# Kernel optimization log

Measured on AMD Instinct MI355X. Metric: run time of the kernel, lower is better.

The kernel has to match this reference:

```python
import jax, jax.numpy as jnp
import numpy as np

DIM = 512
N_HEADS = 8
HEAD_DIM = DIM // N_HEADS
HID = 4 * DIM
N_LEVELS = 3  # len(chunk_sizes)
EPS = 1e-5


def layernorm(x, w, b):
    mu = jnp.mean(x, axis=-1, keepdims=True)
    var = jnp.var(x, axis=-1, keepdims=True)
    return (x - mu) * jax.lax.rsqrt(var + EPS) * w + b


def setup_inputs() -> dict:
    key = jax.random.key(0)
    ks = jax.random.split(key, 12)
    s = 1.0 / np.sqrt(DIM)
    sh = 1.0 / np.sqrt(HID)
    inp = {
        "x": jax.random.normal(ks[0], (4, 2048, DIM), dtype=jnp.float32),
        # torch nn.Linear stores weight as [out, in]; y = x @ W.T
        "Wq": jax.random.uniform(ks[1], (DIM, DIM), minval=-s, maxval=s),
        "Wk": jax.random.uniform(ks[2], (DIM, DIM), minval=-s, maxval=s),
        "Wv": jax.random.uniform(ks[3], (DIM, DIM), minval=-s, maxval=s),
        "Wo": jax.random.uniform(ks[4], (DIM, DIM), minval=-s, maxval=s),
        "ln1_w": jnp.ones((DIM,)), "ln1_b": jnp.zeros((DIM,)),
        "ln2_w": jnp.ones((DIM,)), "ln2_b": jnp.zeros((DIM,)),
        # CMS: per-level MLP, stored as [L, in, out]
        "cms_W1": jax.random.uniform(ks[5], (N_LEVELS, DIM, HID), minval=-s, maxval=s),
        "cms_b1": jnp.zeros((N_LEVELS, HID)),
        "cms_W2": jax.random.uniform(ks[6], (N_LEVELS, HID, DIM), minval=-sh, maxval=sh),
        "cms_b2": jnp.zeros((N_LEVELS, DIM)),
    }
    return inp


def self_mod_attn(h, Wq, Wk, Wv, Wo):
    B, S, _ = h.shape
    def split(y):  # [B,S,dim] -> [B,H,S,D]
        return y.reshape(B, S, N_HEADS, HEAD_DIM).transpose(0, 2, 1, 3)
    Q = split(h @ Wq.T)
    K = split(h @ Wk.T)
    V = split(h @ Wv.T)
    # per-step memory delta, mean over batch: U[h,s,d,k] = mean_b v_t k_t^T
    U = jnp.einsum("bhsd,bhsk->hsdk", V, K) / B
    # memory starts at zero (buffer) and accumulates INCLUDING step t before readout
    M = jnp.cumsum(U, axis=1)  # [H,S,D,D]
    y = jnp.einsum("hsdk,bhsk->bhsd", M, Q)  # readout
    y = y.transpose(0, 2, 1, 3).reshape(B, S, DIM)
    return y @ Wo.T


def cms(h, cms_W1, cms_b1, cms_W2, cms_b2):
    # sequential chain of per-level MLPs (dim -> 4*dim -> dim)
    for l in range(N_LEVELS):
        h = jax.nn.gelu(h @ cms_W1[l] + cms_b1[l]) @ cms_W2[l] + cms_b2[l]
    return h


def reference(x, Wq, Wk, Wv, Wo, ln1_w, ln1_b, ln2_w, ln2_b,
              cms_W1, cms_b1, cms_W2, cms_b2):
    x = x + self_mod_attn(layernorm(x, ln1_w, ln1_b), Wq, Wk, Wv, Wo)
    x = x + cms(layernorm(x, ln2_w, ln2_b), cms_W1, cms_b1, cms_W2, cms_b2)
    return x
```

## Files before the change

### kernel.cpp

```cpp
#include <hip/hip_runtime.h>
#include <hip/hip_bf16.h>
#include <cstdint>
#include <cstddef>

typedef __attribute__((ext_vector_type(8))) short bf16x8;
typedef __attribute__((ext_vector_type(4))) float f32x4;

#define MFMA16(a, b, c) __builtin_amdgcn_mfma_f32_16x16x32_bf16((a), (b), (c), 0, 0, 0)

static __device__ __forceinline__ unsigned short f2bf(float f) {
    union { float f; unsigned u; } v; v.f = f;
    unsigned r = v.u + 0x7fffu + ((v.u >> 16) & 1u);
    return (unsigned short)(r >> 16);
}

static __device__ __forceinline__ float gelu_tanh(float x) {
    float z = 0.7978845608028654f * (x + 0.044715f * x * x * x);
    float a = fabsf(z);
    float e = __expf(-2.0f * a);
    float t = (1.0f - e) / (1.0f + e);
    t = (z < 0.0f) ? -t : t;
    return 0.5f * x * (1.0f + t);
}

static __device__ __forceinline__ void gload16(const void* g, void* l) {
    __builtin_amdgcn_global_load_lds((const __attribute__((address_space(1))) unsigned int*)g,
                                     (__attribute__((address_space(3))) unsigned int*)l,
                                     16, 0, 0);
}

__global__ __launch_bounds__(256) void wcvt_kernel(const float* __restrict__ a, const float* __restrict__ b,
                                                   const float* __restrict__ c, const float* __restrict__ d,
                                                   unsigned short* __restrict__ o) {
    int i = blockIdx.x * 256 + threadIdx.x;
    int idx = i * 4;
    int which = idx >> 18;
    int off = idx & 262143;
    const float* src = (which == 0) ? a : (which == 1) ? b : (which == 2) ? c : d;
    float4 v = *(const float4*)(src + off);
    unsigned long long p = (unsigned long long)f2bf(v.x) | ((unsigned long long)f2bf(v.y) << 16)
                         | ((unsigned long long)f2bf(v.z) << 32) | ((unsigned long long)f2bf(v.w) << 48);
    *(unsigned long long*)(o + idx) = p;
}

__global__ __launch_bounds__(256) void wtrans_kernel(const float* __restrict__ in, unsigned short* __restrict__ out,
                                                     int R, int C) {
    __shared__ float tile[32][33];
    size_t lvl = blockIdx.z;
    in  += lvl * (size_t)R * C;
    out += lvl * (size_t)R * C;
    int c0 = blockIdx.x * 32, r0 = blockIdx.y * 32;
    int tx = threadIdx.x & 31, ty = threadIdx.x >> 5;
    #pragma unroll
    for (int ii = 0; ii < 4; ++ii) {
        int i = ty * 4 + ii;
        tile[i][tx] = in[(size_t)(r0 + i) * C + c0 + tx];
    }
    __syncthreads();
    #pragma unroll
    for (int jj = 0; jj < 4; ++jj) {
        int j = ty * 4 + jj;
        out[(size_t)(c0 + j) * R + r0 + tx] = f2bf(tile[tx][j]);
    }
}

__global__ __launch_bounds__(256) void ln_kernel(const float* __restrict__ x,
                                                 const float* __restrict__ w,
                                                 const float* __restrict__ b,
                                                 unsigned short* __restrict__ out) {
    int tid = threadIdx.x, l = tid & 63, wv = tid >> 6;
    size_t row = (size_t)blockIdx.x * 4 + wv;
    const float* xr = x + row * 512 + l * 8;
    float4 v0 = *(const float4*)xr;
    float4 v1 = *(const float4*)(xr + 4);
    float vv[8] = {v0.x, v0.y, v0.z, v0.w, v1.x, v1.y, v1.z, v1.w};
    float s = 0.f, q = 0.f;
    #pragma unroll
    for (int j = 0; j < 8; ++j) { s += vv[j]; q += vv[j] * vv[j]; }
    #pragma unroll
    for (int off = 1; off < 64; off <<= 1) { s += __shfl_xor(s, off); q += __shfl_xor(q, off); }
    float mu = s * (1.0f / 512.0f);
    float rs = rsqrtf(q * (1.0f / 512.0f) - mu * mu + 1e-5f);
    union { unsigned short us[8]; uint4 u; } pk;
    #pragma unroll
    for (int j = 0; j < 8; ++j)
        pk.us[j] = f2bf((vv[j] - mu) * rs * w[l * 8 + j] + b[l * 8 + j]);
    *(uint4*)(out + row * 512 + l * 8) = pk.u;
}

template<int EPI>
__global__ __launch_bounds__(256) void gemm_bt(
    const unsigned short* __restrict__ A,
    const unsigned short* __restrict__ Bt,
    int K, int N,
    unsigned short* __restrict__ outb,
    float* __restrict__ outf,
    const float* __restrict__ bias,
    const float* __restrict__ resid) {
    __shared__ bf16x8 As[1024];
    __shared__ bf16x8 Bs[1024];
    const int tid = threadIdx.x, l = tid & 63, w = tid >> 6;
    const int m0 = blockIdx.x * 128, n0 = blockIdx.y * 128;
    const int wr = (w >> 1) * 64, wc = (w & 1) * 64;
    const int srow = l >> 3;
    const int scol = ((l & 7) ^ srow) * 8;

    f32x4 acc[4][4] = {};
    const int nkt = K >> 6;
    for (int kt = 0; kt < nkt; ++kt) {
        const unsigned short* Ag = A + (size_t)m0 * K + kt * 64;
        const unsigned short* Bg = Bt + (size_t)n0 * K + kt * 64;
        #pragma unroll
        for (int i = 0; i < 4; ++i) {
            int chunk = i * 4 + w;
            int row = chunk * 8 + srow;
            gload16(Ag + (size_t)row * K + scol, &As[chunk * 64]);
            gload16(Bg + (size_t)row * K + scol, &Bs[chunk * 64]);
        }
        __syncthreads();
        #pragma unroll
        for (int kk = 0; kk < 2; ++kk) {
            bf16x8 af[4], bfr[4];
            #pragma unroll
            for (int mi = 0; mi < 4; ++mi) {
                int r = wr + mi * 16 + (l & 15);
                af[mi] = As[r * 8 + ((kk * 4 + (l >> 4)) ^ (r & 7))];
            }
            #pragma unroll
            for (int ni = 0; ni < 4; ++ni) {
                int r = wc + ni * 16 + (l & 15);
                bfr[ni] = Bs[r * 8 + ((kk * 4 + (l >> 4)) ^ (r & 7))];
            }
            #pragma unroll
            for (int mi = 0; mi < 4; ++mi)
                #pragma unroll
                for (int ni = 0; ni < 4; ++ni)
                    acc[mi][ni] = MFMA16(af[mi], bfr[ni], acc[mi][ni]);
        }
        __syncthreads();
    }
    #pragma unroll
    for (int mi = 0; mi < 4; ++mi)
        #pragma unroll
        for (int ni = 0; ni < 4; ++ni) {
            int col = n0 + wc + ni * 16 + (l & 15);
            #pragma unroll
            for (int r = 0; r < 4; ++r) {
                int row = m0 + wr + mi * 16 + (l >> 4) * 4 + r;
                float v = acc[mi][ni][r];
                size_t idx = (size_t)row * N + col;
                if constexpr (EPI == 0) {
                    outb[idx] = f2bf(v);
                } else if constexpr (EPI == 1) {
                    outf[idx] = v + resid[idx];
                } else if constexpr (EPI == 2) {
                    v += bias[col];
                    outb[idx] = f2bf(gelu_tanh(v));
                } else if constexpr (EPI == 3) {
                    v += bias[col];
                    outb[idx] = f2bf(v);
                } else {
                    v += bias[col];
                    outf[idx] = v + resid[idx];
                }
            }
        }
}

__global__ __launch_bounds__(256) void attn_u_kernel(
    const unsigned short* __restrict__ Km,
    const unsigned short* __restrict__ Vm,
    float* __restrict__ U) {
    const int c = blockIdx.x, h = blockIdx.y;
    const int tid = threadIdx.x, l = tid & 63, w = tid >> 6;
    __shared__ __align__(16) unsigned short Kt[64 * 256];
    __shared__ __align__(16) unsigned short Vt[64 * 256];
    for (int i = 0; i < 8; ++i) {
        int idx = i * 256 + tid;
        int tr = idx >> 3, g = idx & 7;
        int bb = tr >> 6, tl = tr & 63;
        size_t go = (size_t)(bb * 2048 + c * 64 + tl) * 512 + h * 64 + g * 8;
        bf16x8 kv = *(const bf16x8*)(Km + go);
        bf16x8 vv = *(const bf16x8*)(Vm + go);
        #pragma unroll
        for (int j = 0; j < 8; ++j) {
            int d = g * 8 + j;
            int ts = tr ^ ((d & 7) << 3);
            Kt[d * 256 + ts] = (unsigned short)kv[j];
            Vt[d * 256 + ts] = (unsigned short)vv[j];
        }
    }
    __syncthreads();
    const int dr = (w >> 1) * 32, kc = (w & 1) * 32;
    f32x4 acc[2][2] = {};
    #pragma unroll
    for (int kk = 0; kk < 8; ++kk) {
        bf16x8 av[2], bk[2];
        #pragma unroll
        for (int mi = 0; mi < 2; ++mi) {
            int r = dr + mi * 16 + (l & 15);
            av[mi] = *(const bf16x8*)&Vt[r * 256 + ((kk * 32 + (l >> 4) * 8) ^ ((r & 7) << 3))];
        }
        #pragma unroll
        for (int ni = 0; ni < 2; ++ni) {
            int r = kc + ni * 16 + (l & 15);
            bk[ni] = *(const bf16x8*)&Kt[r * 256 + ((kk * 32 + (l >> 4) * 8) ^ ((r & 7) << 3))];
        }
        #pragma unroll
        for (int mi = 0; mi < 2; ++mi)
            #pragma unroll
            for (int ni = 0; ni < 2; ++ni)
                acc[mi][ni] = MFMA16(av[mi], bk[ni], acc[mi][ni]);
    }
    float* Uo = U + (size_t)(h * 32 + c) * 4096;
    #pragma unroll
    for (int mi = 0; mi < 2; ++mi)
        #pragma unroll
        for (int ni = 0; ni < 2; ++ni)
            #pragma unroll
            for (int r = 0; r < 4; ++r) {
                int d = dr + mi * 16 + (l >> 4) * 4 + r;
                int k2 = kc + ni * 16 + (l & 15);
                Uo[d * 64 + k2] = acc[mi][ni][r] * 0.25f;
            }
}

__global__ __launch_bounds__(256) void attn_scan_kernel(const float* __restrict__ U,
                                                        unsigned short* __restrict__ Mx) {
    int e = blockIdx.x * 256 + threadIdx.x;
    int h = blockIdx.y;
    float a = 0.0f;
    for (int c = 0; c < 32; ++c) {
        size_t o = (size_t)(h * 32 + c) * 4096 + e;
        Mx[o] = f2bf(a);
        a += U[o];
    }
}

__global__ __launch_bounds__(256) void attn_y_kernel(
    const unsigned short* __restrict__ Qm,
    const unsigned short* __restrict__ Km,
    const unsigned short* __restrict__ Vm,
    const unsigned short* __restrict__ Mx,
    unsigned short* __restrict__ Y) {
    const int c = blockIdx.x, h = blockIdx.y;
    const int tid = threadIdx.x, l = tid & 63, w = tid >> 6;
    __shared__ __align__(16) unsigned short Vt[64 * 256];
    __shared__ __align__(16) unsigned short Ss[4][64 * 64];

    for (int i = 0; i < 8; ++i) {
        int idx = i * 256 + tid;
        int tr = idx >> 3, g = idx & 7;
        int bb = tr >> 6, tl = tr & 63;
        bf16x8 vv = *(const bf16x8*)(Vm + ((size_t)(bb * 2048 + c * 64 + tl) * 512 + h * 64 + g * 8));
        #pragma unroll
        for (int j = 0; j < 8; ++j) {
            int d = g * 8 + j;
            Vt[d * 256 + (tr ^ ((d & 7) << 3))] = (unsigned short)vv[j];
        }
    }
    __syncthreads();

    f32x4 yacc[4][4] = {};

    bf16x8 qf[2][4];
    #pragma unroll
    for (int kk = 0; kk < 2; ++kk)
        #pragma unroll
        for (int ni = 0; ni < 4; ++ni) {
            int qloc = ni * 16 + (l & 15);
            qf[kk][ni] = *(const bf16x8*)(Qm + ((size_t)(w * 2048 + c * 64 + qloc) * 512
                                                + h * 64 + kk * 32 + (l >> 4) * 8));
        }

    const unsigned short* Mrow = Mx + (size_t)(h * 32 + c) * 4096;
    #pragma unroll
    for (int kk = 0; kk < 2; ++kk) {
        bf16x8 am[4];
        #pragma unroll
        for (int mi = 0; mi < 4; ++mi) {
            int d = mi * 16 + (l & 15);
            am[mi] = *(const bf16x8*)(Mrow + d * 64 + kk * 32 + (l >> 4) * 8);
        }
        #pragma unroll
        for (int mi = 0; mi < 4; ++mi)
            #pragma unroll
            for (int ni = 0; ni < 4; ++ni)
                yacc[mi][ni] = MFMA16(am[mi], qf[kk][ni], yacc[mi][ni]);
    }

    unsigned short* Sw = &Ss[w][0];
    for (int tv = 0; tv < 4; ++tv) {
        #pragma unroll
        for (int th = 0; th < 2; ++th) {
            f32x4 sacc[2][4] = {};
            #pragma unroll
            for (int kk = 0; kk < 2; ++kk) {
                bf16x8 ak[2];
                #pragma unroll
                for (int mi = 0; mi < 2; ++mi) {
                    int tloc = th * 32 + mi * 16 + (l & 15);
                    ak[mi] = *(const bf16x8*)(Km + ((size_t)(tv * 2048 + c * 64 + tloc) * 512
                                                    + h * 64 + kk * 32 + (l >> 4) * 8));
                }
                #pragma unroll
                for (int mi = 0; mi < 2; ++mi)
                    #pragma unroll
                    for (int ni = 0; ni < 4; ++ni)
                        sacc[mi][ni] = MFMA16(ak[mi], qf[kk][ni], sacc[mi][ni]);
            }
            #pragma unroll
            for (int mi = 0; mi < 2; ++mi)
                #pragma unroll
                for (int ni = 0; ni < 4; ++ni) {
                    int tb = th * 32 + mi * 16 + (l >> 4) * 4;
                    int qcol = ni * 16 + (l & 15);
                    unsigned long long p = 0;
                    #pragma unroll
                    for (int r = 0; r < 4; ++r) {
                        float v = (tb + r <= qcol) ? sacc[mi][ni][r] * 0.25f : 0.0f;
                        p |= ((unsigned long long)f2bf(v)) << (16 * r);
                    }
                    int ts = tb ^ ((qcol & 7) << 3);
                    *(unsigned long long*)(Sw + qcol * 64 + ts) = p;
                }
        }
        #pragma unroll
        for (int kk2 = 0; kk2 < 2; ++kk2) {
            bf16x8 av[4], bs[4];
            #pragma unroll
            for (int mi = 0; mi < 4; ++mi) {
                int d = mi * 16 + (l & 15);
                av[mi] = *(const bf16x8*)&Vt[d * 256 + ((tv * 64 + kk2 * 32 + (l >> 4) * 8) ^ ((d & 7) << 3))];
            }
            #pragma unroll
            for (int ni = 0; ni < 4; ++ni) {
                int q = ni * 16 + (l & 15);
                bs[ni] = *(const bf16x8*)&Sw[q * 64 + ((kk2 * 32 + (l >> 4) * 8) ^ ((q & 7) << 3))];
            }
            #pragma unroll
            for (int mi = 0; mi < 4; ++mi)
                #pragma unroll
                for (int ni = 0; ni < 4; ++ni)
                    yacc[mi][ni] = MFMA16(av[mi], bs[ni], yacc[mi][ni]);
        }
    }

    #pragma unroll
    for (int mi = 0; mi < 4; ++mi)
        #pragma unroll
        for (int ni = 0; ni < 4; ++ni) {
            int qloc = ni * 16 + (l & 15);
            int d0 = mi * 16 + (l >> 4) * 4;
            unsigned long long p = 0;
            #pragma unroll
            for (int r = 0; r < 4; ++r)
                p |= ((unsigned long long)f2bf(yacc[mi][ni][r])) << (16 * r);
            *(unsigned long long*)(Y + ((size_t)(w * 2048 + c * 64 + qloc) * 512 + h * 64 + d0)) = p;
        }
}

extern "C" void kernel_launch(void* const* d_in, const int* in_sizes, int n_in,
                              void* d_out, int out_size, void* d_ws, size_t ws_size,
                              hipStream_t stream) {
    const float* x    = (const float*)d_in[0];
    const float* Wq   = (const float*)d_in[1];
    const float* Wk   = (const float*)d_in[2];
    const float* Wv   = (const float*)d_in[3];
    const float* Wo   = (const float*)d_in[4];
    const float* ln1w = (const float*)d_in[5];
    const float* ln1b = (const float*)d_in[6];
    const float* ln2w = (const float*)d_in[7];
    const float* ln2b = (const float*)d_in[8];
    const float* W1   = (const float*)d_in[9];
    const float* b1   = (const float*)d_in[10];
    const float* W2   = (const float*)d_in[11];
    const float* b2   = (const float*)d_in[12];
    float* out = (float*)d_out;
    char* ws = (char*)d_ws;
    const size_t MB = 1024 * 1024;
    unsigned short* Wqb = (unsigned short*)(ws + 0 * MB);
    unsigned short* W1t = (unsigned short*)(ws + 2 * MB);
    unsigned short* W2t = (unsigned short*)(ws + 8 * MB);
    unsigned short* hb  = (unsigned short*)(ws + 14 * MB);
    unsigned short* Qb  = (unsigned short*)(ws + 22 * MB);
    unsigned short* Kb  = (unsigned short*)(ws + 30 * MB);
    unsigned short* Vb  = (unsigned short*)(ws + 38 * MB);
    unsigned short* Yb  = (unsigned short*)(ws + 46 * MB);
    unsigned short* tb  = (unsigned short*)(ws + 22 * MB);
    float*          x2  = (float*)(ws + 54 * MB);
    float*          U   = (float*)(ws + 70 * MB);
    unsigned short* Mx  = (unsigned short*)(ws + 74 * MB);

    wcvt_kernel<<<1024, 256, 0, stream>>>(Wq, Wk, Wv, Wo, Wqb);
    wtrans_kernel<<<dim3(64, 16, 3), 256, 0, stream>>>(W1, W1t, 512, 2048);
    wtrans_kernel<<<dim3(16, 64, 3), 256, 0, stream>>>(W2, W2t, 2048, 512);

    ln_kernel<<<2048, 256, 0, stream>>>(x, ln1w, ln1b, hb);

    dim3 gq(64, 4);
    gemm_bt<0><<<gq, 256, 0, stream>>>(hb, Wqb + 0 * 262144, 512, 512, Qb, nullptr, nullptr, nullptr);
    gemm_bt<0><<<gq, 256, 0, stream>>>(hb, Wqb + 1 * 262144, 512, 512, Kb, nullptr, nullptr, nullptr);
    gemm_bt<0><<<gq, 256, 0, stream>>>(hb, Wqb + 2 * 262144, 512, 512, Vb, nullptr, nullptr, nullptr);

    attn_u_kernel<<<dim3(32, 8), 256, 0, stream>>>(Kb, Vb, U);
    attn_scan_kernel<<<dim3(16, 8), 256, 0, stream>>>(U, Mx);
    attn_y_kernel<<<dim3(32, 8), 256, 0, stream>>>(Qb, Kb, Vb, Mx, Yb);

    gemm_bt<1><<<gq, 256, 0, stream>>>(Yb, Wqb + 3 * 262144, 512, 512, nullptr, x2, nullptr, x);

    ln_kernel<<<2048, 256, 0, stream>>>(x2, ln2w, ln2b, hb);

    dim3 g1(64, 16);
    for (int lvl = 0; lvl < 3; ++lvl) {
        gemm_bt<2><<<g1, 256, 0, stream>>>(hb, W1t + (size_t)lvl * 1048576, 512, 2048,
                                           tb, nullptr, b1 + lvl * 2048, nullptr);
        if (lvl < 2)
            gemm_bt<3><<<gq, 256, 0, stream>>>(tb, W2t + (size_t)lvl * 1048576, 2048, 512,
                                               hb, nullptr, b2 + lvl * 512, nullptr);
        else
            gemm_bt<4><<<gq, 256, 0, stream>>>(tb, W2t + (size_t)lvl * 1048576, 2048, 512,
                                               nullptr, out, b2 + lvl * 512, x2);
    }
}
```

Baseline: 325.6 us.

## Double-buffer GEMM LDS, fuse QKV projection, split-K the down projection

After: 283.6 us. 12.9% less time.

```diff
diff --git a/kernel.cpp b/kernel.cpp
--- a/kernel.cpp
+++ b/kernel.cpp
@@ -92,44 +92,58 @@
 __global__ __launch_bounds__(256) void gemm_bt(
     const unsigned short* __restrict__ A,
     const unsigned short* __restrict__ Bt,
-    int K, int N,
+    int K, int lda, int ldb, int N,
     unsigned short* __restrict__ outb,
     float* __restrict__ outf,
     const float* __restrict__ bias,
-    const float* __restrict__ resid) {
-    __shared__ bf16x8 As[1024];
-    __shared__ bf16x8 Bs[1024];
+    const float* __restrict__ resid,
+    size_t planeStride) {
+    __shared__ bf16x8 As[2][1024];
+    __shared__ bf16x8 Bs[2][1024];
     const int tid = threadIdx.x, l = tid & 63, w = tid >> 6;
     const int m0 = blockIdx.x * 128, n0 = blockIdx.y * 128;
     const int wr = (w >> 1) * 64, wc = (w & 1) * 64;
     const int srow = l >> 3;
     const int scol = ((l & 7) ^ srow) * 8;
 
-    f32x4 acc[4][4] = {};
+    if constexpr (EPI == 5) {
+        size_t z = blockIdx.z;
+        A    += z * (size_t)K;
+        Bt   += z * (size_t)K;
+        outf += z * planeStride;
+    }
+
     const int nkt = K >> 6;
-    for (int kt = 0; kt < nkt; ++kt) {
-        const unsigned short* Ag = A + (size_t)m0 * K + kt * 64;
-        const unsigned short* Bg = Bt + (size_t)n0 * K + kt * 64;
+    auto stage = [&](int buf, int kt) {
+        const unsigned short* Ag = A + (size_t)m0 * lda + kt * 64;
+        const unsigned short* Bg = Bt + (size_t)n0 * ldb + kt * 64;
         #pragma unroll
         for (int i = 0; i < 4; ++i) {
             int chunk = i * 4 + w;
             int row = chunk * 8 + srow;
-            gload16(Ag + (size_t)row * K + scol, &As[chunk * 64]);
-            gload16(Bg + (size_t)row * K + scol, &Bs[chunk * 64]);
-        }
-        __syncthreads();
+            gload16(Ag + (size_t)row * lda + scol, &As[buf][chunk * 64]);
+            gload16(Bg + (size_t)row * ldb + scol, &Bs[buf][chunk * 64]);
+        }
+    };
+
+    f32x4 acc[4][4] = {};
+    stage(0, 0);
+    __syncthreads();
+    int cur = 0;
+    for (int kt = 0; kt < nkt; ++kt) {
+        if (kt + 1 < nkt) stage(cur ^ 1, kt + 1);
         #pragma unroll
         for (int kk = 0; kk < 2; ++kk) {
             bf16x8 af[4], bfr[4];
             #pragma unroll
             for (int mi = 0; mi < 4; ++mi) {
                 int r = wr + mi * 16 + (l & 15);
-                af[mi] = As[r * 8 + ((kk * 4 + (l >> 4)) ^ (r & 7))];
+                af[mi] = As[cur][r * 8 + ((kk * 4 + (l >> 4)) ^ (r & 7))];
             }
             #pragma unroll
             for (int ni = 0; ni < 4; ++ni) {
                 int r = wc + ni * 16 + (l & 15);
-                bfr[ni] = Bs[r * 8 + ((kk * 4 + (l >> 4)) ^ (r & 7))];
+                bfr[ni] = Bs[cur][r * 8 + ((kk * 4 + (l >> 4)) ^ (r & 7))];
             }
             #pragma unroll
             for (int mi = 0; mi < 4; ++mi)
@@ -138,7 +152,9 @@
                     acc[mi][ni] = MFMA16(af[mi], bfr[ni], acc[mi][ni]);
         }
         __syncthreads();
-    }
+        cur ^= 1;
+    }
+
     #pragma unroll
     for (int mi = 0; mi < 4; ++mi)
         #pragma unroll
@@ -159,17 +175,42 @@
                 } else if constexpr (EPI == 3) {
                     v += bias[col];
                     outb[idx] = f2bf(v);
-                } else {
+                } else if constexpr (EPI == 4) {
                     v += bias[col];
                     outf[idx] = v + resid[idx];
+                } else {
+                    outf[idx] = v;
                 }
             }
         }
 }
 
+template<bool FINAL>
+__global__ __launch_bounds__(256) void reduce_down(const float* __restrict__ P,
+                                                   const float* __restrict__ bias,
+                                                   const float* __restrict__ resid,
+                                                   unsigned short* __restrict__ outb,
+                                                   float* __restrict__ outf) {
+    size_t i = ((size_t)blockIdx.x * 256 + threadIdx.x) * 4;
+    int col = (int)(i & 511);
+    const float4 a = *(const float4*)(P + i);
+    const float4 b = *(const float4*)(P + 4194304 + i);
+    const float4 bs = *(const float4*)(bias + col);
+    float v0 = a.x + b.x + bs.x, v1 = a.y + b.y + bs.y;
+    float v2 = a.z + b.z + bs.z, v3 = a.w + b.w + bs.w;
+    if constexpr (FINAL) {
+        const float4 r = *(const float4*)(resid + i);
+        float4 o = {v0 + r.x, v1 + r.y, v2 + r.z, v3 + r.w};
+        *(float4*)(outf + i) = o;
+    } else {
+        unsigned long long p = (unsigned long long)f2bf(v0) | ((unsigned long long)f2bf(v1) << 16)
+                             | ((unsigned long long)f2bf(v2) << 32) | ((unsigned long long)f2bf(v3) << 48);
+        *(unsigned long long*)(outb + i) = p;
+    }
+}
+
 __global__ __launch_bounds__(256) void attn_u_kernel(
-    const unsigned short* __restrict__ Km,
-    const unsigned short* __restrict__ Vm,
+    const unsigned short* __restrict__ QKV,
     float* __restrict__ U) {
     const int c = blockIdx.x, h = blockIdx.y;
     const int tid = threadIdx.x, l = tid & 63, w = tid >> 6;
@@ -179,9 +220,9 @@
         int idx = i * 256 + tid;
         int tr = idx >> 3, g = idx & 7;
         int bb = tr >> 6, tl = tr & 63;
-        size_t go = (size_t)(bb * 2048 + c * 64 + tl) * 512 + h * 64 + g * 8;
-        bf16x8 kv = *(const bf16x8*)(Km + go);
-        bf16x8 vv = *(const bf16x8*)(Vm + go);
+        size_t go = (size_t)(bb * 2048 + c * 64 + tl) * 1536 + h * 64 + g * 8;
+        bf16x8 kv = *(const bf16x8*)(QKV + go + 512);
+        bf16x8 vv = *(const bf16x8*)(QKV + go + 1024);
         #pragma unroll
         for (int j = 0; j < 8; ++j) {
             int d = g * 8 + j;
@@ -238,9 +279,7 @@
 }
 
 __global__ __launch_bounds__(256) void attn_y_kernel(
-    const unsigned short* __restrict__ Qm,
-    const unsigned short* __restrict__ Km,
-    const unsigned short* __restrict__ Vm,
+    const unsigned short* __restrict__ QKV,
     const unsigned short* __restrict__ Mx,
     unsigned short* __restrict__ Y) {
     const int c = blockIdx.x, h = blockIdx.y;
@@ -252,7 +291,7 @@
         int idx = i * 256 + tid;
         int tr = idx >> 3, g = idx & 7;
         int bb = tr >> 6, tl = tr & 63;
-        bf16x8 vv = *(const bf16x8*)(Vm + ((size_t)(bb * 2048 + c * 64 + tl) * 512 + h * 64 + g * 8));
+        bf16x8 vv = *(const bf16x8*)(QKV + ((size_t)(bb * 2048 + c * 64 + tl) * 1536 + 1024 + h * 64 + g * 8));
         #pragma unroll
         for (int j = 0; j < 8; ++j) {
             int d = g * 8 + j;
@@ -269,7 +308,7 @@
         #pragma unroll
         for (int ni = 0; ni < 4; ++ni) {
             int qloc = ni * 16 + (l & 15);
-            qf[kk][ni] = *(const bf16x8*)(Qm + ((size_t)(w * 2048 + c * 64 + qloc) * 512
+            qf[kk][ni] = *(const bf16x8*)(QKV + ((size_t)(w * 2048 + c * 64 + qloc) * 1536
                                                 + h * 64 + kk * 32 + (l >> 4) * 8));
         }
 
@@ -300,8 +339,8 @@
                 #pragma unroll
                 for (int mi = 0; mi < 2; ++mi) {
                     int tloc = th * 32 + mi * 16 + (l & 15);
-                    ak[mi] = *(const bf16x8*)(Km + ((size_t)(tv * 2048 + c * 64 + tloc) * 512
-                                                    + h * 64 + kk * 32 + (l >> 4) * 8));
+                    ak[mi] = *(const bf16x8*)(QKV + ((size_t)(tv * 2048 + c * 64 + tloc) * 1536
+                                                    + 512 + h * 64 + kk * 32 + (l >> 4) * 8));
                 }
                 #pragma unroll
                 for (int mi = 0; mi < 2; ++mi)
@@ -379,18 +418,19 @@
     float* out = (float*)d_out;
     char* ws = (char*)d_ws;
     const size_t MB = 1024 * 1024;
-    unsigned short* Wqb = (unsigned short*)(ws + 0 * MB);
-    unsigned short* W1t = (unsigned short*)(ws + 2 * MB);
-    unsigned short* W2t = (unsigned short*)(ws + 8 * MB);
-    unsigned short* hb  = (unsigned short*)(ws + 14 * MB);
-    unsigned short* Qb  = (unsigned short*)(ws + 22 * MB);
-    unsigned short* Kb  = (unsigned short*)(ws + 30 * MB);
-    unsigned short* Vb  = (unsigned short*)(ws + 38 * MB);
-    unsigned short* Yb  = (unsigned short*)(ws + 46 * MB);
-    unsigned short* tb  = (unsigned short*)(ws + 22 * MB);
-    float*          x2  = (float*)(ws + 54 * MB);
-    float*          U   = (float*)(ws + 70 * MB);
-    unsigned short* Mx  = (unsigned short*)(ws + 74 * MB);
+    unsigned short* Wqb  = (unsigned short*)(ws + 0 * MB);
+    unsigned short* W1t  = (unsigned short*)(ws + 2 * MB);
+    unsigned short* W2t  = (unsigned short*)(ws + 8 * MB);
+    unsigned short* hb   = (unsigned short*)(ws + 14 * MB);
+    unsigned short* QKVb = (unsigned short*)(ws + 22 * MB);
+    unsigned short* Yb   = (unsigned short*)(ws + 46 * MB);
+    unsigned short* tb   = (unsigned short*)(ws + 22 * MB);
+    float*          x2   = (float*)(ws + 54 * MB);
+    float*          U    = (float*)(ws + 70 * MB);
+    unsigned short* Mx   = (unsigned short*)(ws + 74 * MB);
+    float*          P    = (float*)(ws + 76 * MB);
+
+    const bool splitk = ws_size >= (size_t)108 * MB;
 
     wcvt_kernel<<<1024, 256, 0, stream>>>(Wq, Wk, Wv, Wo, Wqb);
     wtrans_kernel<<<dim3(64, 16, 3), 256, 0, stream>>>(W1, W1t, 512, 2048);
@@ -398,28 +438,40 @@
 
     ln_kernel<<<2048, 256, 0, stream>>>(x, ln1w, ln1b, hb);
 
-    dim3 gq(64, 4);
-    gemm_bt<0><<<gq, 256, 0, stream>>>(hb, Wqb + 0 * 262144, 512, 512, Qb, nullptr, nullptr, nullptr);
-    gemm_bt<0><<<gq, 256, 0, stream>>>(hb, Wqb + 1 * 262144, 512, 512, Kb, nullptr, nullptr, nullptr);
-    gemm_bt<0><<<gq, 256, 0, stream>>>(hb, Wqb + 2 * 262144, 512, 512, Vb, nullptr, nullptr, nullptr);
-
-    attn_u_kernel<<<dim3(32, 8), 256, 0, stream>>>(Kb, Vb, U);
+    gemm_bt<0><<<dim3(64, 12), 256, 0, stream>>>(hb, Wqb, 512, 512, 512, 1536,
+                                                 QKVb, nullptr, nullptr, nullptr, 0);
+
+    attn_u_kernel<<<dim3(32, 8), 256, 0, stream>>>(QKVb, U);
     attn_scan_kernel<<<dim3(16, 8), 256, 0, stream>>>(U, Mx);
-    attn_y_kernel<<<dim3(32, 8), 256, 0, stream>>>(Qb, Kb, Vb, Mx, Yb);
-
-    gemm_bt<1><<<gq, 256, 0, stream>>>(Yb, Wqb + 3 * 262144, 512, 512, nullptr, x2, nullptr, x);
+    attn_y_kernel<<<dim3(32, 8), 256, 0, stream>>>(QKVb, Mx, Yb);
+
+    gemm_bt<1><<<dim3(64, 4), 256, 0, stream>>>(Yb, Wqb + 3 * 262144, 512, 512, 512, 512,
+                                                nullptr, x2, nullptr, x, 0);
 
     ln_kernel<<<2048, 256, 0, stream>>>(x2, ln2w, ln2b, hb);
 
-    dim3 g1(64, 16);
     for (int lvl = 0; lvl < 3; ++lvl) {
-        gemm_bt<2><<<g1, 256, 0, stream>>>(hb, W1t + (size_t)lvl * 1048576, 512, 2048,
-                                           tb, nullptr, b1 + lvl * 2048, nullptr);
-        if (lvl < 2)
-            gemm_bt<3><<<gq, 256, 0, stream>>>(tb, W2t + (size_t)lvl * 1048576, 2048, 512,
-                                               hb, nullptr, b2 + lvl * 512, nullptr);
-        else
-            gemm_bt<4><<<gq, 256, 0, stream>>>(tb, W2t + (size_t)lvl * 1048576, 2048, 512,
-                                               nullptr, out, b2 + lvl * 512, x2);
-    }
-}
+        gemm_bt<2><<<dim3(64, 16), 256, 0, stream>>>(hb, W1t + (size_t)lvl * 1048576,
+                                                     512, 512, 512, 2048,
+                                                     tb, nullptr, b1 + lvl * 2048, nullptr, 0);
+        if (splitk) {
+            gemm_bt<5><<<dim3(64, 4, 2), 256, 0, stream>>>(tb, W2t + (size_t)lvl * 1048576,
+                                                           1024, 2048, 2048, 512,
+                                                           nullptr, P, nullptr, nullptr,
+                                                           (size_t)8192 * 512);
+            if (lvl < 2)
+                reduce_down<false><<<4096, 256, 0, stream>>>(P, b2 + lvl * 512, nullptr, hb, nullptr);
+            else
+                reduce_down<true><<<4096, 256, 0, stream>>>(P, b2 + lvl * 512, x2, nullptr, out);
+        } else {
+            if (lvl < 2)
+                gemm_bt<3><<<dim3(64, 4), 256, 0, stream>>>(tb, W2t + (size_t)lvl * 1048576,
+                                                            2048, 2048, 2048, 512,
+                                                            hb, nullptr, b2 + lvl * 512, nullptr, 0);
+            else
+                gemm_bt<4><<<dim3(64, 4), 256, 0, stream>>>(tb, W2t + (size_t)lvl * 1048576,
+                                                            2048, 2048, 2048, 512,
+                                                            nullptr, out, b2 + lvl * 512, x2, 0);
+        }
+    }
+}
```
